# Performance work log

Hardware: AMD Instinct MI355X
Metric: run time of the kernel (lower is better)

## Reference

```python
import jax, jax.numpy as jnp
import numpy as np

N = 100000   # nodes
E = 625000   # edges
H = 128      # hidden dim
G = 64       # graphs in batch
HOPS = 5
EPS = 1e-5


def _gelu(x):
    return jax.nn.gelu(x, approximate=False)  # torch nn.GELU default (exact erf)


def _bn(x, g, b):
    # BatchNorm1d in training mode: batch statistics, biased variance
    m = jnp.mean(x, axis=0)
    v = jnp.var(x, axis=0)
    return (x - m) * jax.lax.rsqrt(v + EPS) * g + b


def _ffnn(x, W1, b1, W2, b2):
    # Linear -> GELU -> Linear -> GELU
    return _gelu(_gelu(x @ W1 + b1) @ W2 + b2)


def _vn_mlp(x, W1, b1, g1, be1, W2, b2, g2, be2):
    # Linear -> BN -> GELU -> Linear -> BN -> GELU
    h = _gelu(_bn(x @ W1 + b1, g1, be1))
    return _gelu(_bn(h @ W2 + b2, g2, be2))


def _gcn(x, W, b, src, dst):
    # PyG GCNConv: xW, symmetric-normalized aggregation over edges w/ self loops, + bias
    h = x @ W
    deg = jax.ops.segment_sum(jnp.ones_like(src, dtype=h.dtype), dst, num_segments=N)
    dinv = jax.lax.rsqrt(jnp.maximum(deg, 1.0))  # deg >= 1 due to self loops
    norm = dinv[src] * dinv[dst]                 # [E+N]
    out = jax.ops.segment_sum(h[src] * norm[:, None], dst, num_segments=N)
    return out + b


def _forward(x, edge_index, batch, pre_W1, pre_b1, pre_W2, pre_b2, conv_W, conv_b,
             bn_g, bn_b, ffn_W1, ffn_b1, ffn_W2, ffn_b2, vn_W1, vn_b1, vn_g1, vn_be1,
             vn_W2, vn_b2, vn_g2, vn_be2, vn_emb, post_W1, post_b1, post_W2, post_b2):
    loop = jnp.arange(N)
    src = jnp.concatenate([edge_index[0], loop])
    dst = jnp.concatenate([edge_index[1], loop])

    x = _ffnn(x.astype(jnp.float32), pre_W1, pre_b1, pre_W2, pre_b2)
    vn = jnp.broadcast_to(vn_emb[0], (G, H))  # vn(zeros(num_graphs))

    counts = jax.ops.segment_sum(jnp.ones((N,), x.dtype), batch, num_segments=G)
    inv_counts = 1.0 / jnp.maximum(counts, 1.0)

    for i in range(HOPS):
        x = x + vn[batch]
        x = _gcn(x, conv_W[i], conv_b[i], src, dst) + x
        x = _bn(x, bn_g[i], bn_b[i])
        x = _ffnn(x, ffn_W1[i], ffn_b1[i], ffn_W2[i], ffn_b2[i]) + x
        # dropout p=0.0 -> identity
        if i < HOPS - 1:
            pooled = jax.ops.segment_sum(x, batch, num_segments=G) * inv_counts[:, None]
            vn = vn + pooled
            vn = _vn_mlp(vn, vn_W1[i], vn_b1[i], vn_g1[i], vn_be1[i],
                         vn_W2[i], vn_b2[i], vn_g2[i], vn_be2[i])

    x = jax.ops.segment_sum(x, batch, num_segments=G)  # global_add_pool
    return _ffnn(x, post_W1, post_b1, post_W2, post_b2)


def setup_inputs():
    key = jax.random.key(0)
    ks = iter(jax.random.split(key, 40))
    def nrm(shape, s=0.05):
        return jax.random.normal(next(ks), shape, dtype=jnp.float32) * s
    d = {}
    d["x"] = jax.random.normal(next(ks), (N, H), dtype=jnp.float32)
    d["edge_index"] = jax.random.randint(next(ks), (2, E), 0, N)
    d["batch"] = jnp.sort(jax.random.randint(next(ks), (N,), 0, G))
    d["pre_W1"] = nrm((H, 2 * H)); d["pre_b1"] = jnp.zeros((2 * H,), jnp.float32)
    d["pre_W2"] = nrm((2 * H, H)); d["pre_b2"] = jnp.zeros((H,), jnp.float32)
    d["conv_W"] = nrm((HOPS, H, H)); d["conv_b"] = jnp.zeros((HOPS, H), jnp.float32)
    d["bn_g"] = jnp.ones((HOPS, H), jnp.float32); d["bn_b"] = jnp.zeros((HOPS, H), jnp.float32)
    d["ffn_W1"] = nrm((HOPS, H, 2 * H)); d["ffn_b1"] = jnp.zeros((HOPS, 2 * H), jnp.float32)
    d["ffn_W2"] = nrm((HOPS, 2 * H, H)); d["ffn_b2"] = jnp.zeros((HOPS, H), jnp.float32)
    d["vn_W1"] = nrm((HOPS - 1, H, 2 * H)); d["vn_b1"] = jnp.zeros((HOPS - 1, 2 * H), jnp.float32)
    d["vn_g1"] = jnp.ones((HOPS - 1, 2 * H), jnp.float32); d["vn_be1"] = jnp.zeros((HOPS - 1, 2 * H), jnp.float32)
    d["vn_W2"] = nrm((HOPS - 1, 2 * H, H)); d["vn_b2"] = jnp.zeros((HOPS - 1, H), jnp.float32)
    d["vn_g2"] = jnp.ones((HOPS - 1, H), jnp.float32); d["vn_be2"] = jnp.zeros((HOPS - 1, H), jnp.float32)
    d["vn_emb"] = nrm((1, H))
    d["post_W1"] = nrm((H, 2 * H)); d["post_b1"] = jnp.zeros((2 * H,), jnp.float32)
    d["post_W2"] = nrm((2 * H, H)); d["post_b2"] = jnp.zeros((H,), jnp.float32)
    return d


def reference(x, edge_index, batch, pre_W1, pre_b1, pre_W2, pre_b2, conv_W, conv_b,
              bn_g, bn_b, ffn_W1, ffn_b1, ffn_W2, ffn_b2, vn_W1, vn_b1, vn_g1, vn_be1,
              vn_W2, vn_b2, vn_g2, vn_be2, vn_emb, post_W1, post_b1, post_W2, post_b2):
    return _forward(x, edge_index, batch, pre_W1, pre_b1, pre_W2, pre_b2, conv_W, conv_b,
                    bn_g, bn_b, ffn_W1, ffn_b1, ffn_W2, ffn_b2, vn_W1, vn_b1, vn_g1, vn_be1,
                    vn_W2, vn_b2, vn_g2, vn_be2, vn_emb, post_W1, post_b1, post_W2, post_b2)
```

## Files before the change

kernel.cpp:

```cpp
#include <hip/hip_runtime.h>
#include <math.h>

#define H 128
#define H2 256
#define LDK 72
#define LDC 136
#define LDHW 136
#define FFN_SMEM (H2 * LDK)

typedef __attribute__((ext_vector_type(8))) short short8;
typedef __attribute__((ext_vector_type(4))) float floatx4;

__device__ __forceinline__ float gelu_f(float x) {
  float t = 1.59576912161f * x * fmaf(0.044715f, x * x, 1.0f);
  return x / (1.0f + __expf(-t));
}

__device__ __forceinline__ unsigned short f2b(float f) {
  union { float f; unsigned u; } c; c.f = f;
  unsigned r = c.u + 0x7fffu + ((c.u >> 16) & 1u);
  return (unsigned short)(r >> 16);
}

__device__ __forceinline__ float b2f(unsigned short u) {
  union { unsigned u; float f; } c; c.u = ((unsigned)u) << 16; return c.f;
}

__device__ __forceinline__ short8 pack8(floatx4 a, floatx4 b) {
  union { short8 v; unsigned short s[8]; } u;
  u.s[0] = f2b(a.x); u.s[1] = f2b(a.y); u.s[2] = f2b(a.z); u.s[3] = f2b(a.w);
  u.s[4] = f2b(b.x); u.s[5] = f2b(b.y); u.s[6] = f2b(b.z); u.s[7] = f2b(b.w);
  return u.v;
}

__global__ __launch_bounds__(256) void transpose_w(const float* __restrict__ W, unsigned short* __restrict__ WT,
                                                   int K, int Ncol, int total) {
  int i = blockIdx.x * 256 + threadIdx.x;
  if (i >= total) return;
  int kn = K * Ncol;
  int b = i / kn, r = i - b * kn;
  int k = r / Ncol, n = r - k * Ncol;
  WT[b * kn + n * K + k] = f2b(W[i]);
}


__global__ __launch_bounds__(256) void hist_kernel(int* __restrict__ cnt, const int* __restrict__ dst, int E) {
  int i = blockIdx.x * 256 + threadIdx.x;
  if (i < E) atomicAdd(&cnt[dst[i]], 1);
}

__global__ __launch_bounds__(256) void scan_a(const int* __restrict__ cnt, int* __restrict__ row_ptr,
                                              int* __restrict__ blockSum, float* __restrict__ dinv, int N) {
  __shared__ int ls[256];
  int t = threadIdx.x;
  int idx = blockIdx.x * 1024 + t * 4;
  int4 v = make_int4(0, 0, 0, 0);
  if (idx + 3 < N) v = *(const int4*)&cnt[idx];
  else {
    if (idx + 0 < N) v.x = cnt[idx + 0];
    if (idx + 1 < N) v.y = cnt[idx + 1];
    if (idx + 2 < N) v.z = cnt[idx + 2];
    if (idx + 3 < N) v.w = cnt[idx + 3];
  }
  if (idx + 0 < N) dinv[idx + 0] = rsqrtf((float)v.x + 1.0f);
  if (idx + 1 < N) dinv[idx + 1] = rsqrtf((float)v.y + 1.0f);
  if (idx + 2 < N) dinv[idx + 2] = rsqrtf((float)v.z + 1.0f);
  if (idx + 3 < N) dinv[idx + 3] = rsqrtf((float)v.w + 1.0f);
  int s = v.x + v.y + v.z + v.w;
  ls[t] = s;
  __syncthreads();
  for (int off = 1; off < 256; off <<= 1) {
    int a = (t >= off) ? ls[t - off] : 0;
    __syncthreads();
    ls[t] += a;
    __syncthreads();
  }
  int p = ls[t] - s;
  if (t == 255) blockSum[blockIdx.x] = ls[255];
  if (idx + 0 < N) row_ptr[idx + 0] = p;  p += v.x;
  if (idx + 1 < N) row_ptr[idx + 1] = p;  p += v.y;
  if (idx + 2 < N) row_ptr[idx + 2] = p;  p += v.z;
  if (idx + 3 < N) row_ptr[idx + 3] = p;
}

__global__ __launch_bounds__(1024) void scan_b(const int* __restrict__ blockSum, int* __restrict__ blockOff,
                                               int nb, int* __restrict__ row_ptr, int N, int E) {
  __shared__ int ls[1024];
  int t = threadIdx.x;
  int s = (t < nb) ? blockSum[t] : 0;
  ls[t] = s;
  __syncthreads();
  for (int off = 1; off < 1024; off <<= 1) {
    int a = (t >= off) ? ls[t - off] : 0;
    __syncthreads();
    ls[t] += a;
    __syncthreads();
  }
  if (t < nb) blockOff[t] = ls[t] - s;
  if (t == 0) row_ptr[N] = E;
}

__global__ __launch_bounds__(256) void scan_c(int* __restrict__ row_ptr, const int* __restrict__ blockOff, int N) {
  int t = threadIdx.x;
  int idx = blockIdx.x * 1024 + t * 4;
  int off = blockOff[blockIdx.x];
  if (off == 0) return;
  if (idx + 3 < N) {
    int4 v = *(const int4*)&row_ptr[idx];
    v.x += off; v.y += off; v.z += off; v.w += off;
    *(int4*)&row_ptr[idx] = v;
  } else {
    if (idx + 0 < N) row_ptr[idx + 0] += off;
    if (idx + 1 < N) row_ptr[idx + 1] += off;
    if (idx + 2 < N) row_ptr[idx + 2] += off;
    if (idx + 3 < N) row_ptr[idx + 3] += off;
  }
}

__global__ __launch_bounds__(256) void build_csr_kernel(const int* __restrict__ src, const int* __restrict__ dst,
                                                        const int* __restrict__ row_ptr, int* __restrict__ cursor,
                                                        const float* __restrict__ dinv,
                                                        int* __restrict__ csr_src, float* __restrict__ csr_norm,
                                                        int E) {
  int i = blockIdx.x * 256 + threadIdx.x;
  if (i < E) {
    int s = src[i], d = dst[i];
    int pos = row_ptr[d] + atomicAdd(&cursor[d], 1);
    csr_src[pos] = s;
    csr_norm[pos] = dinv[s] * dinv[d];
  }
}


__global__ __launch_bounds__(256) void count_kernel(float* counts, const int* __restrict__ batch, int N, int G) {
  __shared__ float hist[256];
  int t = threadIdx.x;
  if (t < G) hist[t] = 0.f;
  __syncthreads();
  int i0 = (blockIdx.x * 256 + t) * 16;
  int cur = -1; float run = 0.f;
  for (int j = 0; j < 16; j++) {
    int i = i0 + j;
    if (i < N) {
      int b = batch[i];
      if (b == cur) run += 1.f;
      else { if (cur >= 0) atomicAdd(&hist[cur], run); cur = b; run = 1.f; }
    }
  }
  if (cur >= 0) atomicAdd(&hist[cur], run);
  __syncthreads();
  if (t < G && hist[t] != 0.f) atomicAdd(&counts[t], hist[t]);
}

__global__ __launch_bounds__(256) void vn_init_kernel(float* vn, const float* __restrict__ emb, int n) {
  int i = blockIdx.x * 256 + threadIdx.x;
  if (i < n) vn[i] = emb[i & (H - 1)];
}

__global__ __launch_bounds__(256) void gather_agg(const unsigned short* __restrict__ h, const int* __restrict__ csr_src,
                                                  const float* __restrict__ csr_norm, const int* __restrict__ row_ptr,
                                                  const float* __restrict__ dinv, const float* __restrict__ vn,
                                                  const int* __restrict__ batch, const float* __restrict__ bias,
                                                  float* __restrict__ x, float* __restrict__ stats, int N) {
  __shared__ float sred[4 * H];
  __shared__ float qred[4 * H];
  int w = threadIdx.x >> 6, lane = threadIdx.x & 63;
  int c = lane * 2;
  float2 bi = *(const float2*)&bias[c];
  float s0t = 0.f, s1t = 0.f, q0t = 0.f, q1t = 0.f;
  int base = blockIdx.x * 32 + w * 8;
  for (int j = 0; j < 8; j++) {
    int node = base + j;
    if (node >= N) break;
    int b = batch[node];
    float di = dinv[node];
    float2 xo = *(const float2*)&x[(long)node * H + c];
    float2 vv = *(const float2*)&vn[b * H + c];
    unsigned hv = *(const unsigned*)&h[(long)node * H + c];
    int beg = row_ptr[node], end = row_ptr[node + 1];
    float ax = b2f((unsigned short)hv) * di * di;
    float ay = b2f((unsigned short)(hv >> 16)) * di * di;
    for (int e = beg; e < end; e += 8) {
      int si[8]; float wg[8]; unsigned u[8];
#pragma unroll
      for (int i = 0; i < 8; i++) {
        int ee = e + i;
        bool in = ee < end;
        int idx = in ? ee : beg;
        si[i] = csr_src[idx];
        wg[i] = in ? csr_norm[idx] : 0.f;
      }
#pragma unroll
      for (int i = 0; i < 8; i++) u[i] = *(const unsigned*)&h[(long)si[i] * H + c];
#pragma unroll
      for (int i = 0; i < 8; i++) {
        ax += b2f((unsigned short)u[i]) * wg[i];
        ay += b2f((unsigned short)(u[i] >> 16)) * wg[i];
      }
    }
    float rx = ax + xo.x + vv.x + bi.x;
    float ry = ay + xo.y + vv.y + bi.y;
    *(float2*)&x[(long)node * H + c] = make_float2(rx, ry);
    s0t += rx; q0t += rx * rx;
    s1t += ry; q1t += ry * ry;
  }
  sred[w * H + c] = s0t; sred[w * H + c + 1] = s1t;
  qred[w * H + c] = q0t; qred[w * H + c + 1] = q1t;
  __syncthreads();
  int t = threadIdx.x;
  if (t < H) {
    float s = sred[t] + sred[H + t] + sred[2 * H + t] + sred[3 * H + t];
    if (s != 0.f) atomicAdd(&stats[t], s);
  } else {
    int cc = t - H;
    float q = qred[cc] + qred[H + cc] + qred[2 * H + cc] + qred[3 * H + cc];
    if (q != 0.f) atomicAdd(&stats[H + cc], q);
  }
}

__global__ __launch_bounds__(128) void bn_finalize_kernel(const float* __restrict__ stats, const float* __restrict__ g,
                                                          const float* __restrict__ b, float* __restrict__ scsh,
                                                          float invN) {
  int c = threadIdx.x;
  float m = stats[c] * invN;
  float v = stats[H + c] * invN - m * m;
  float sc = rsqrtf(v + 1e-5f) * g[c];
  scsh[c] = sc;
  scsh[H + c] = b[c] - m * sc;
}

__global__ __launch_bounds__(256) void pool_kernel(float* __restrict__ pooled, const float* __restrict__ x,
                                                   const int* __restrict__ batch, int N) {
  int c = threadIdx.x & 127;
  int slab = threadIdx.x >> 7;
  int r0 = blockIdx.x * 128 + slab;
  float acc = 0.f;
  int cur = -1;
  for (int k = 0; k < 64; k++) {
    int r = r0 + k * 2;
    if (r >= N) break;
    int b = batch[r];
    if (b != cur) {
      if (cur >= 0) atomicAdd(&pooled[cur * H + c], acc);
      cur = b; acc = 0.f;
    }
    acc += x[(long)r * H + c];
  }
  if (cur >= 0) atomicAdd(&pooled[cur * H + c], acc);
}

__global__ __launch_bounds__(256) void conv_gemm(const float* __restrict__ x, const unsigned short* __restrict__ BT,
                                                 const float* __restrict__ vn, const int* __restrict__ batch,
                                                 unsigned short* __restrict__ h16, int M) {
  __shared__ unsigned short Bs[H * LDC];
  int tid = threadIdx.x;
  int lane = tid & 63, w = tid >> 6;
  int row0 = blockIdx.x * 64;
  int mrow = lane & 15, quad = lane >> 4, cn = lane & 15;
  int arow = row0 + w * 16 + mrow;
  bool rin = arow < M;
  int b = rin ? batch[arow] : 0;

#pragma unroll
  for (int j = 0; j < 8; j++) {
    int chunk = j * 256 + tid;
    int n = chunk >> 4, k8 = (chunk & 15) * 8;
    *(short8*)&Bs[n * LDC + k8] = *(const short8*)&BT[(long)n * H + k8];
  }

  short8 af[4];
#pragma unroll
  for (int k0 = 0; k0 < 4; k0++) {
    int kb = k0 * 32 + quad * 8;
    floatx4 a0 = (floatx4)0.f, a1 = (floatx4)0.f;
    if (rin) {
      a0 = *(const floatx4*)&x[(long)arow * H + kb] + *(const floatx4*)&vn[b * H + kb];
      a1 = *(const floatx4*)&x[(long)arow * H + kb + 4] + *(const floatx4*)&vn[b * H + kb + 4];
    }
    af[k0] = pack8(a0, a1);
  }
  __syncthreads();

#pragma unroll
  for (int t = 0; t < 8; t++) {
    floatx4 a = (floatx4)0.f;
#pragma unroll
    for (int k0 = 0; k0 < 4; k0++) {
      int kb = k0 * 32 + quad * 8;
      short8 bf = *(const short8*)&Bs[(t * 16 + mrow) * LDC + kb];
      a = __builtin_amdgcn_mfma_f32_16x16x32_bf16(af[k0], bf, a, 0, 0, 0);
    }
    int c = t * 16 + cn;
#pragma unroll
    for (int i = 0; i < 4; i++) {
      int r = row0 + w * 16 + quad * 4 + i;
      if (r < M) h16[(long)r * H + c] = f2b(a[i]);
    }
  }
}

template <int BNRES>
__global__ __launch_bounds__(256) void ffn_fused(const float* __restrict__ A,
                                                 const unsigned short* __restrict__ W1T, const float* __restrict__ b1,
                                                 const unsigned short* __restrict__ W2T, const float* __restrict__ b2,
                                                 const float* __restrict__ scsh,
                                                 float* __restrict__ C, int M) {
  __shared__ unsigned short smem[FFN_SMEM];
  unsigned short* Bs1 = smem;
  unsigned short* Bs2 = smem + 4 * 16 * LDHW;

  int tid = threadIdx.x;
  int lane = tid & 63, w = tid >> 6;
  unsigned short* HsW = smem + w * 16 * LDHW;
  int row0 = blockIdx.x * 64;
  int mrow = lane & 15, quad = lane >> 4, cn = lane & 15;
  int arow = row0 + w * 16 + mrow;
  bool rin = arow < M;

  short8 af[4];
#pragma unroll
  for (int k0 = 0; k0 < 4; k0++) {
    int kb = k0 * 32 + quad * 8;
    floatx4 a0 = (floatx4)0.f, a1 = (floatx4)0.f;
    if (rin) {
      a0 = *(const floatx4*)&A[(long)arow * H + kb];
      a1 = *(const floatx4*)&A[(long)arow * H + kb + 4];
      if (BNRES) {
        a0 = a0 * *(const floatx4*)&scsh[kb] + *(const floatx4*)&scsh[H + kb];
        a1 = a1 * *(const floatx4*)&scsh[kb + 4] + *(const floatx4*)&scsh[H + kb + 4];
      }
    }
    af[k0] = pack8(a0, a1);
  }

  floatx4 acc1[16];
#pragma unroll
  for (int t = 0; t < 16; t++) acc1[t] = (floatx4)0.f;

  for (int ks = 0; ks < 2; ks++) {
    if (ks > 0) __syncthreads();
#pragma unroll
    for (int j = 0; j < 8; j++) {
      int chunk = j * 256 + tid;
      int n = chunk >> 3, k8 = (chunk & 7) * 8;
      *(short8*)&Bs1[n * LDK + k8] = *(const short8*)&W1T[(long)n * H + ks * 64 + k8];
    }
    __syncthreads();
#pragma unroll
    for (int t = 0; t < 16; t++) {
      int kb = quad * 8;
      short8 bf0 = *(const short8*)&Bs1[(t * 16 + mrow) * LDK + kb];
      acc1[t] = __builtin_amdgcn_mfma_f32_16x16x32_bf16(af[ks * 2], bf0, acc1[t], 0, 0, 0);
      short8 bf1 = *(const short8*)&Bs1[(t * 16 + mrow) * LDK + 32 + kb];
      acc1[t] = __builtin_amdgcn_mfma_f32_16x16x32_bf16(af[ks * 2 + 1], bf1, acc1[t], 0, 0, 0);
    }
  }
  __syncthreads();

  short8 hf[8];
#pragma unroll
  for (int half = 0; half < 2; half++) {
#pragma unroll
    for (int t = 0; t < 8; t++) {
      int tt = half * 8 + t;
      int cg = tt * 16 + cn;
      int cl = t * 16 + cn;
      float bb = b1[cg];
#pragma unroll
      for (int i = 0; i < 4; i++) {
        int r = quad * 4 + i;
        HsW[r * LDHW + cl] = f2b(gelu_f(acc1[tt][i] + bb));
      }
    }
#pragma unroll
    for (int k0 = 0; k0 < 4; k0++)
      hf[half * 4 + k0] = *(const short8*)&HsW[mrow * LDHW + k0 * 32 + quad * 8];
  }

#pragma unroll
  for (int j = 0; j < 4; j++) {
    int chunk = j * 256 + tid;
    int n = chunk >> 3, k8 = (chunk & 7) * 8;
    *(short8*)&Bs2[n * LDK + k8] = *(const short8*)&W2T[(long)n * H2 + k8];
  }
  __syncthreads();

  floatx4 acc2[8];
#pragma unroll
  for (int t = 0; t < 8; t++) acc2[t] = (floatx4)0.f;

  for (int ks = 0; ks < 4; ks++) {
    if (ks > 0) {
      __syncthreads();
#pragma unroll
      for (int j = 0; j < 4; j++) {
        int chunk = j * 256 + tid;
        int n = chunk >> 3, k8 = (chunk & 7) * 8;
        *(short8*)&Bs2[n * LDK + k8] = *(const short8*)&W2T[(long)n * H2 + ks * 64 + k8];
      }
      __syncthreads();
    }
    int kk = ks * 2;
#pragma unroll
    for (int t = 0; t < 8; t++) {
      int kb0 = quad * 8;
      short8 bf0 = *(const short8*)&Bs2[(t * 16 + mrow) * LDK + kb0];
      acc2[t] = __builtin_amdgcn_mfma_f32_16x16x32_bf16(hf[kk], bf0, acc2[t], 0, 0, 0);
      short8 bf1 = *(const short8*)&Bs2[(t * 16 + mrow) * LDK + 32 + kb0];
      acc2[t] = __builtin_amdgcn_mfma_f32_16x16x32_bf16(hf[kk + 1], bf1, acc2[t], 0, 0, 0);
    }
  }

#pragma unroll
  for (int t = 0; t < 8; t++) {
    int c = t * 16 + cn;
    float bb = b2[c];
    float rsc = 0.f, rsh = 0.f;
    if (BNRES) { rsc = scsh[c]; rsh = scsh[H + c]; }
#pragma unroll
    for (int i = 0; i < 4; i++) {
      int r = row0 + w * 16 + quad * 4 + i;
      if (r < M) {
        long off = (long)r * H + c;
        float v = gelu_f(acc2[t][i] + bb);
        if (BNRES) v += C[off] * rsc + rsh;
        C[off] = v;
      }
    }
  }
}

template <int BN, int UVN>
__global__ __launch_bounds__(256) void mlp64_l1(const float* __restrict__ vn, const float* __restrict__ pooled,
                                                const float* __restrict__ counts,
                                                const float* __restrict__ W1, const float* __restrict__ b1,
                                                const float* __restrict__ g1, const float* __restrict__ be1,
                                                float* __restrict__ h1) {
  __shared__ float u[64 * H];
  __shared__ float red[8 * 64];
  int t = threadIdx.x;
  for (int idx = t; idx < 64 * H; idx += 256) {
    float v = pooled[idx];
    if (UVN) v = vn[idx] + v / fmaxf(counts[idx >> 7], 1.0f);
    u[idx] = v;
  }
  __syncthreads();
  int tc = t & 63, tg = t >> 6;
  int c = blockIdx.x * 64 + tc;
  float acc[16];
  float bj = b1[c];
#pragma unroll
  for (int g = 0; g < 16; g++) acc[g] = bj;
  for (int k0 = 0; k0 < H; k0 += 4) {
    float w0 = W1[(k0 + 0) * H2 + c];
    float w1 = W1[(k0 + 1) * H2 + c];
    float w2 = W1[(k0 + 2) * H2 + c];
    float w3 = W1[(k0 + 3) * H2 + c];
#pragma unroll
    for (int g = 0; g < 16; g++) {
      float4 v = *(const float4*)&u[(tg * 16 + g) * H + k0];
      acc[g] += v.x * w0 + v.y * w1 + v.z * w2 + v.w * w3;
    }
  }
  float sc = 1.f, sh = 0.f;
  if (BN) {
    float s = 0.f, s2 = 0.f;
#pragma unroll
    for (int g = 0; g < 16; g++) { s += acc[g]; s2 += acc[g] * acc[g]; }
    red[tg * 64 + tc] = s;
    red[256 + tg * 64 + tc] = s2;
    __syncthreads();
    float st = red[tc] + red[64 + tc] + red[128 + tc] + red[192 + tc];
    float st2 = red[256 + tc] + red[320 + tc] + red[384 + tc] + red[448 + tc];
    float m = st * (1.f / 64.f);
    float var = st2 * (1.f / 64.f) - m * m;
    sc = rsqrtf(var + 1e-5f) * g1[c];
    sh = be1[c] - m * sc;
  }
#pragma unroll
  for (int g = 0; g < 16; g++) h1[(tg * 16 + g) * H2 + c] = gelu_f(acc[g] * sc + sh);
}

template <int BN>
__global__ __launch_bounds__(256) void mlp64_l2(const float* __restrict__ h1,
                                                const float* __restrict__ W2, const float* __restrict__ b2,
                                                const float* __restrict__ g2, const float* __restrict__ be2,
                                                float* __restrict__ outp) {
  __shared__ float red[8 * 64];
  int t = threadIdx.x;
  int tc = t & 63, tg = t >> 6;
  int c = blockIdx.x * 64 + tc;
  float acc[16];
  float bj = b2[c];
#pragma unroll
  for (int g = 0; g < 16; g++) acc[g] = bj;
  for (int k0 = 0; k0 < H2; k0 += 4) {
    float w0 = W2[(k0 + 0) * H + c];
    float w1 = W2[(k0 + 1) * H + c];
    float w2 = W2[(k0 + 2) * H + c];
    float w3 = W2[(k0 + 3) * H + c];
#pragma unroll
    for (int g = 0; g < 16; g++) {
      float4 v = *(const float4*)&h1[(tg * 16 + g) * H2 + k0];
      acc[g] += v.x * w0 + v.y * w1 + v.z * w2 + v.w * w3;
    }
  }
  float sc = 1.f, sh = 0.f;
  if (BN) {
    float s = 0.f, s2 = 0.f;
#pragma unroll
    for (int g = 0; g < 16; g++) { s += acc[g]; s2 += acc[g] * acc[g]; }
    red[tg * 64 + tc] = s;
    red[256 + tg * 64 + tc] = s2;
    __syncthreads();
    float st = red[tc] + red[64 + tc] + red[128 + tc] + red[192 + tc];
    float st2 = red[256 + tc] + red[320 + tc] + red[384 + tc] + red[448 + tc];
    float m = st * (1.f / 64.f);
    float var = st2 * (1.f / 64.f) - m * m;
    sc = rsqrtf(var + 1e-5f) * g2[c];
    sh = be2[c] - m * sc;
  }
#pragma unroll
  for (int g = 0; g < 16; g++) outp[(tg * 16 + g) * H + c] = gelu_f(acc[g] * sc + sh);
}


extern "C" void kernel_launch(void* const* d_in, const int* in_sizes, int n_in,
                              void* d_out, int out_size, void* d_ws, size_t ws_size,
                              hipStream_t stream) {
  const float* x_in   = (const float*)d_in[0];
  const int*   edge   = (const int*)d_in[1];
  const int*   batch  = (const int*)d_in[2];
  const float* pre_W1 = (const float*)d_in[3];
  const float* pre_b1 = (const float*)d_in[4];
  const float* pre_W2 = (const float*)d_in[5];
  const float* pre_b2 = (const float*)d_in[6];
  const float* conv_W = (const float*)d_in[7];
  const float* conv_b = (const float*)d_in[8];
  const float* bn_g   = (const float*)d_in[9];
  const float* bn_b   = (const float*)d_in[10];
  const float* ffn_W1 = (const float*)d_in[11];
  const float* ffn_b1 = (const float*)d_in[12];
  const float* ffn_W2 = (const float*)d_in[13];
  const float* ffn_b2 = (const float*)d_in[14];
  const float* vn_W1  = (const float*)d_in[15];
  const float* vn_b1  = (const float*)d_in[16];
  const float* vn_g1  = (const float*)d_in[17];
  const float* vn_be1 = (const float*)d_in[18];
  const float* vn_W2  = (const float*)d_in[19];
  const float* vn_b2  = (const float*)d_in[20];
  const float* vn_g2  = (const float*)d_in[21];
  const float* vn_be2 = (const float*)d_in[22];
  const float* vn_emb = (const float*)d_in[23];
  const float* post_W1= (const float*)d_in[24];
  const float* post_b1= (const float*)d_in[25];
  const float* post_W2= (const float*)d_in[26];
  const float* post_b2= (const float*)d_in[27];
  float* out = (float*)d_out;

  const int N    = in_sizes[2];
  const int E    = in_sizes[1] / 2;
  const int G    = out_size / H;
  const int HOPS = in_sizes[7] / (H * H);
  const int NH   = N * H;

  float* w = (float*)d_ws;
  float* buf_x  = w;  w += NH;
  float* buf_t  = w;  w += N * H2;
  unsigned short* buf_h16 = (unsigned short*)buf_t;
  float* dinv   = w;  w += N;
  float* counts = w;  w += G;
  float* stats  = w;  w += 2 * H;
  float* scsh   = w;  w += 2 * H;
  float* pooled = w;  w += G * H;
  float* vn     = w;  w += G * H;
  float* mlp_h1 = w;  w += G * H2;
  float* csr_norm = w; w += E;
  int* iw = (int*)w;
  int* cnt      = iw;  iw += N;
  int* row_ptr  = iw;  iw += N + 1;
  int* cursor   = iw;  iw += N;
  int* csr_src  = iw;  iw += E;
  int* blockSum = iw;  iw += 1024;
  int* blockOff = iw;  iw += 1024;
  unsigned short* wt = (unsigned short*)iw;
  unsigned short* preW1T = wt;  wt += H * H2;
  unsigned short* preW2T = wt;  wt += H2 * H;
  unsigned short* convT  = wt;  wt += HOPS * H * H;
  unsigned short* ffn1T  = wt;  wt += HOPS * H * H2;
  unsigned short* ffn2T  = wt;  wt += HOPS * H2 * H;

  const int* src = edge;
  const int* dst = edge + E;

  int gE  = (E + 255) / 256;
  int gM  = (N + 63) / 64;
  int nb  = (N + 1023) / 1024;
  float invN = 1.0f / (float)N;

  transpose_w<<<(H * H2 + 255) / 256, 256, 0, stream>>>(pre_W1, preW1T, H, H2, H * H2);
  transpose_w<<<(H2 * H + 255) / 256, 256, 0, stream>>>(pre_W2, preW2T, H2, H, H2 * H);
  transpose_w<<<(HOPS * H * H + 255) / 256, 256, 0, stream>>>(conv_W, convT, H, H, HOPS * H * H);
  transpose_w<<<(HOPS * H * H2 + 255) / 256, 256, 0, stream>>>(ffn_W1, ffn1T, H, H2, HOPS * H * H2);
  transpose_w<<<(HOPS * H2 * H + 255) / 256, 256, 0, stream>>>(ffn_W2, ffn2T, H2, H, HOPS * H2 * H);

  hipMemsetAsync(cnt, 0, N * sizeof(int), stream);
  hist_kernel<<<gE, 256, 0, stream>>>(cnt, dst, E);
  scan_a<<<nb, 256, 0, stream>>>(cnt, row_ptr, blockSum, dinv, N);
  scan_b<<<1, 1024, 0, stream>>>(blockSum, blockOff, nb, row_ptr, N, E);
  scan_c<<<nb, 256, 0, stream>>>(row_ptr, blockOff, N);
  hipMemsetAsync(cursor, 0, N * sizeof(int), stream);
  build_csr_kernel<<<gE, 256, 0, stream>>>(src, dst, row_ptr, cursor, dinv, csr_src, csr_norm, E);

  hipMemsetAsync(counts, 0, G * sizeof(float), stream);
  count_kernel<<<(N + 256 * 16 - 1) / (256 * 16), 256, 0, stream>>>(counts, batch, N, G);
  vn_init_kernel<<<(G * H + 255) / 256, 256, 0, stream>>>(vn, vn_emb, G * H);

  ffn_fused<0><<<gM, 256, 0, stream>>>(x_in, preW1T, pre_b1, preW2T, pre_b2, nullptr, buf_x, N);

  for (int i = 0; i < HOPS; i++) {
    conv_gemm<<<gM, 256, 0, stream>>>(buf_x, convT + i * H * H, vn, batch, buf_h16, N);
    hipMemsetAsync(stats, 0, 2 * H * sizeof(float), stream);
    gather_agg<<<(N + 31) / 32, 256, 0, stream>>>(buf_h16, csr_src, csr_norm, row_ptr, dinv, vn, batch,
                                                  conv_b + i * H, buf_x, stats, N);
    bn_finalize_kernel<<<1, 128, 0, stream>>>(stats, bn_g + i * H, bn_b + i * H, scsh, invN);
    ffn_fused<1><<<gM, 256, 0, stream>>>(buf_x, ffn1T + i * H * H2, ffn_b1 + i * H2,
                                         ffn2T + i * H2 * H, ffn_b2 + i * H, scsh, buf_x, N);
    if (i < HOPS - 1) {
      hipMemsetAsync(pooled, 0, G * H * sizeof(float), stream);
      pool_kernel<<<(N + 127) / 128, 256, 0, stream>>>(pooled, buf_x, batch, N);
      mlp64_l1<1, 1><<<H2 / 64, 256, 0, stream>>>(vn, pooled, counts,
                                                  vn_W1 + i * H * H2, vn_b1 + i * H2, vn_g1 + i * H2, vn_be1 + i * H2,
                                                  mlp_h1);
      mlp64_l2<1><<<H / 64, 256, 0, stream>>>(mlp_h1, vn_W2 + i * H2 * H, vn_b2 + i * H, vn_g2 + i * H, vn_be2 + i * H, vn);
    }
  }

  hipMemsetAsync(pooled, 0, G * H * sizeof(float), stream);
  pool_kernel<<<(N + 127) / 128, 256, 0, stream>>>(pooled, buf_x, batch, N);
  mlp64_l1<0, 0><<<H2 / 64, 256, 0, stream>>>(nullptr, pooled, nullptr, post_W1, post_b1, nullptr, nullptr, mlp_h1);
  mlp64_l2<0><<<H / 64, 256, 0, stream>>>(mlp_h1, post_W2, post_b2, nullptr, nullptr, out);
}
```

Baseline: 1.877 ms.

## Make FFN kernel persistent with resident weights and fused graph pooling

Replaces the per-tile FFN kernel with a persistent 1024-thread kernel that loads both weight matrices into LDS once per block. Each wave then loops over 16-row tiles, computing the first GEMM in column pairs and feeding the GELU output straight into the second GEMM through a small per-wave scratch area. Graph mean-pooling is folded into the FFN epilogue using shuffle reductions and atomics, which removes the separate pool kernel and its re-read of x. The costs are a large LDS footprint that limits each CU to one block, and more atomics when a tile spans two graphs.

```diff
diff --git a/kernel.cpp b/kernel.cpp
--- a/kernel.cpp
+++ b/kernel.cpp
@@ -3,10 +3,7 @@
 
 #define H 128
 #define H2 256
-#define LDK 72
 #define LDC 136
-#define LDHW 136
-#define FFN_SMEM (H2 * LDK)
 
 typedef __attribute__((ext_vector_type(8))) short short8;
 typedef __attribute__((ext_vector_type(4))) float floatx4;
@@ -229,26 +226,6 @@
   scsh[H + c] = b[c] - m * sc;
 }
 
-__global__ __launch_bounds__(256) void pool_kernel(float* __restrict__ pooled, const float* __restrict__ x,
-                                                   const int* __restrict__ batch, int N) {
-  int c = threadIdx.x & 127;
-  int slab = threadIdx.x >> 7;
-  int r0 = blockIdx.x * 128 + slab;
-  float acc = 0.f;
-  int cur = -1;
-  for (int k = 0; k < 64; k++) {
-    int r = r0 + k * 2;
-    if (r >= N) break;
-    int b = batch[r];
-    if (b != cur) {
-      if (cur >= 0) atomicAdd(&pooled[cur * H + c], acc);
-      cur = b; acc = 0.f;
-    }
-    acc += x[(long)r * H + c];
-  }
-  if (cur >= 0) atomicAdd(&pooled[cur * H + c], acc);
-}
-
 __global__ __launch_bounds__(256) void conv_gemm(const float* __restrict__ x, const unsigned short* __restrict__ BT,
                                                  const float* __restrict__ vn, const int* __restrict__ batch,
                                                  unsigned short* __restrict__ h16, int M) {
@@ -299,132 +276,114 @@
   }
 }
 
-template <int BNRES>
-__global__ __launch_bounds__(256) void ffn_fused(const float* __restrict__ A,
-                                                 const unsigned short* __restrict__ W1T, const float* __restrict__ b1,
-                                                 const unsigned short* __restrict__ W2T, const float* __restrict__ b2,
-                                                 const float* __restrict__ scsh,
-                                                 float* __restrict__ C, int M) {
-  __shared__ unsigned short smem[FFN_SMEM];
-  unsigned short* Bs1 = smem;
-  unsigned short* Bs2 = smem + 4 * 16 * LDHW;
-
+template <int BNRES, int POOL>
+__global__ __launch_bounds__(1024) void ffn_persist(const float* __restrict__ A,
+                                                    const unsigned short* __restrict__ W1T, const float* __restrict__ b1,
+                                                    const unsigned short* __restrict__ W2T, const float* __restrict__ b2,
+                                                    const float* __restrict__ scsh,
+                                                    float* __restrict__ C, float* __restrict__ pooled,
+                                                    const int* __restrict__ batch, int M) {
+  __shared__ unsigned short lds[78848];
   int tid = threadIdx.x;
+#pragma unroll
+  for (int j = 0; j < 4; j++) {
+    int idx = j * 1024 + tid;
+    int n = idx >> 4, k8 = (idx & 15) * 8;
+    *(short8*)&lds[n * 136 + k8] = *(const short8*)&W1T[n * 128 + k8];
+  }
+#pragma unroll
+  for (int j = 0; j < 4; j++) {
+    int idx = j * 1024 + tid;
+    int n = idx >> 5, k8 = (idx & 31) * 8;
+    *(short8*)&lds[34816 + n * 264 + k8] = *(const short8*)&W2T[n * 256 + k8];
+  }
+  __syncthreads();
+
   int lane = tid & 63, w = tid >> 6;
-  unsigned short* HsW = smem + w * 16 * LDHW;
-  int row0 = blockIdx.x * 64;
   int mrow = lane & 15, quad = lane >> 4, cn = lane & 15;
-  int arow = row0 + w * 16 + mrow;
-  bool rin = arow < M;
-
-  short8 af[4];
-#pragma unroll
-  for (int k0 = 0; k0 < 4; k0++) {
-    int kb = k0 * 32 + quad * 8;
-    floatx4 a0 = (floatx4)0.f, a1 = (floatx4)0.f;
-    if (rin) {
-      a0 = *(const floatx4*)&A[(long)arow * H + kb];
-      a1 = *(const floatx4*)&A[(long)arow * H + kb + 4];
-      if (BNRES) {
-        a0 = a0 * *(const floatx4*)&scsh[kb] + *(const floatx4*)&scsh[H + kb];
-        a1 = a1 * *(const floatx4*)&scsh[kb + 4] + *(const floatx4*)&scsh[H + kb + 4];
+  unsigned short* scr = &lds[68608 + w * 640];
+  int TT = (M + 15) >> 4;
+  int stride = (int)(gridDim.x << 4);
+
+  for (int tile = blockIdx.x * 16 + w; tile < TT; tile += stride) {
+    int row0 = tile << 4;
+    int arow = row0 + mrow;
+    bool rin = arow < M;
+
+    short8 af[4];
+#pragma unroll
+    for (int k0 = 0; k0 < 4; k0++) {
+      int kb = k0 * 32 + quad * 8;
+      floatx4 a0 = (floatx4)0.f, a1 = (floatx4)0.f;
+      if (rin) {
+        a0 = *(const floatx4*)&A[(long)arow * H + kb];
+        a1 = *(const floatx4*)&A[(long)arow * H + kb + 4];
+        if (BNRES) {
+          a0 = a0 * *(const floatx4*)&scsh[kb] + *(const floatx4*)&scsh[H + kb];
+          a1 = a1 * *(const floatx4*)&scsh[kb + 4] + *(const floatx4*)&scsh[H + kb + 4];
+        }
       }
-    }
-    af[k0] = pack8(a0, a1);
-  }
-
-  floatx4 acc1[16];
-#pragma unroll
-  for (int t = 0; t < 16; t++) acc1[t] = (floatx4)0.f;
-
-  for (int ks = 0; ks < 2; ks++) {
-    if (ks > 0) __syncthreads();
-#pragma unroll
-    for (int j = 0; j < 8; j++) {
-      int chunk = j * 256 + tid;
-      int n = chunk >> 3, k8 = (chunk & 7) * 8;
-      *(short8*)&Bs1[n * LDK + k8] = *(const short8*)&W1T[(long)n * H + ks * 64 + k8];
-    }
-    __syncthreads();
-#pragma unroll
-    for (int t = 0; t < 16; t++) {
-      int kb = quad * 8;
-      short8 bf0 = *(const short8*)&Bs1[(t * 16 + mrow) * LDK + kb];
-      acc1[t] = __builtin_amdgcn_mfma_f32_16x16x32_bf16(af[ks * 2], bf0, acc1[t], 0, 0, 0);
-      short8 bf1 = *(const short8*)&Bs1[(t * 16 + mrow) * LDK + 32 + kb];
-      acc1[t] = __builtin_amdgcn_mfma_f32_16x16x32_bf16(af[ks * 2 + 1], bf1, acc1[t], 0, 0, 0);
-    }
-  }
-  __syncthreads();
-
-  short8 hf[8];
-#pragma unroll
-  for (int half = 0; half < 2; half++) {
+      af[k0] = pack8(a0, a1);
+    }
+
+    floatx4 acc2[8];
+#pragma unroll
+    for (int t = 0; t < 8; t++) acc2[t] = (floatx4)0.f;
+
+#pragma unroll
+    for (int p = 0; p < 8; p++) {
+#pragma unroll
+      for (int u = 0; u < 2; u++) {
+        int t = p * 2 + u;
+        floatx4 a = (floatx4)0.f;
+#pragma unroll
+        for (int k = 0; k < 4; k++) {
+          short8 bf = *(const short8*)&lds[(t * 16 + mrow) * 136 + k * 32 + quad * 8];
+          a = __builtin_amdgcn_mfma_f32_16x16x32_bf16(af[k], bf, a, 0, 0, 0);
+        }
+        float bb = b1[t * 16 + cn];
+#pragma unroll
+        for (int i = 0; i < 4; i++)
+          scr[(quad * 4 + i) * 40 + u * 16 + cn] = f2b(gelu_f(a[i] + bb));
+      }
+      short8 hf = *(const short8*)&scr[mrow * 40 + quad * 8];
+#pragma unroll
+      for (int ct = 0; ct < 8; ct++) {
+        short8 bf = *(const short8*)&lds[34816 + (ct * 16 + mrow) * 264 + p * 32 + quad * 8];
+        acc2[ct] = __builtin_amdgcn_mfma_f32_16x16x32_bf16(hf, bf, acc2[ct], 0, 0, 0);
+      }
+    }
+
+    int g0 = 0; bool same = true;
+    if (POOL) {
+      int rl = row0 + 15; if (rl >= M) rl = M - 1;
+      g0 = batch[row0];
+      same = (batch[rl] == g0);
+    }
 #pragma unroll
     for (int t = 0; t < 8; t++) {
-      int tt = half * 8 + t;
-      int cg = tt * 16 + cn;
-      int cl = t * 16 + cn;
-      float bb = b1[cg];
+      int c = t * 16 + cn;
+      float bb = b2[c];
+      float rsc = 0.f, rsh = 0.f;
+      if (BNRES) { rsc = scsh[c]; rsh = scsh[H + c]; }
+      float s = 0.f;
 #pragma unroll
       for (int i = 0; i < 4; i++) {
-        int r = quad * 4 + i;
-        HsW[r * LDHW + cl] = f2b(gelu_f(acc1[tt][i] + bb));
+        int r = row0 + quad * 4 + i;
+        float v = 0.f;
+        if (r < M) {
+          long off = (long)r * H + c;
+          v = gelu_f(acc2[t][i] + bb);
+          if (BNRES) v += C[off] * rsc + rsh;
+          C[off] = v;
+          if (POOL && !same) atomicAdd(&pooled[batch[r] * H + c], v);
+        }
+        s += v;
       }
-    }
-#pragma unroll
-    for (int k0 = 0; k0 < 4; k0++)
-      hf[half * 4 + k0] = *(const short8*)&HsW[mrow * LDHW + k0 * 32 + quad * 8];
-  }
-
-#pragma unroll
-  for (int j = 0; j < 4; j++) {
-    int chunk = j * 256 + tid;
-    int n = chunk >> 3, k8 = (chunk & 7) * 8;
-    *(short8*)&Bs2[n * LDK + k8] = *(const short8*)&W2T[(long)n * H2 + k8];
-  }
-  __syncthreads();
-
-  floatx4 acc2[8];
-#pragma unroll
-  for (int t = 0; t < 8; t++) acc2[t] = (floatx4)0.f;
-
-  for (int ks = 0; ks < 4; ks++) {
-    if (ks > 0) {
-      __syncthreads();
-#pragma unroll
-      for (int j = 0; j < 4; j++) {
-        int chunk = j * 256 + tid;
-        int n = chunk >> 3, k8 = (chunk & 7) * 8;
-        *(short8*)&Bs2[n * LDK + k8] = *(const short8*)&W2T[(long)n * H2 + ks * 64 + k8];
-      }
-      __syncthreads();
-    }
-    int kk = ks * 2;
-#pragma unroll
-    for (int t = 0; t < 8; t++) {
-      int kb0 = quad * 8;
-      short8 bf0 = *(const short8*)&Bs2[(t * 16 + mrow) * LDK + kb0];
-      acc2[t] = __builtin_amdgcn_mfma_f32_16x16x32_bf16(hf[kk], bf0, acc2[t], 0, 0, 0);
-      short8 bf1 = *(const short8*)&Bs2[(t * 16 + mrow) * LDK + 32 + kb0];
-      acc2[t] = __builtin_amdgcn_mfma_f32_16x16x32_bf16(hf[kk + 1], bf1, acc2[t], 0, 0, 0);
-    }
-  }
-
-#pragma unroll
-  for (int t = 0; t < 8; t++) {
-    int c = t * 16 + cn;
-    float bb = b2[c];
-    float rsc = 0.f, rsh = 0.f;
-    if (BNRES) { rsc = scsh[c]; rsh = scsh[H + c]; }
-#pragma unroll
-    for (int i = 0; i < 4; i++) {
-      int r = row0 + w * 16 + quad * 4 + i;
-      if (r < M) {
-        long off = (long)r * H + c;
-        float v = gelu_f(acc2[t][i] + bb);
-        if (BNRES) v += C[off] * rsc + rsh;
-        C[off] = v;
+      if (POOL && same) {
+        s += __shfl_xor(s, 16);
+        s += __shfl_xor(s, 32);
+        if (quad == 0) atomicAdd(&pooled[g0 * H + c], s);
       }
     }
   }
@@ -616,7 +575,8 @@
   count_kernel<<<(N + 256 * 16 - 1) / (256 * 16), 256, 0, stream>>>(counts, batch, N, G);
   vn_init_kernel<<<(G * H + 255) / 256, 256, 0, stream>>>(vn, vn_emb, G * H);
 
-  ffn_fused<0><<<gM, 256, 0, stream>>>(x_in, preW1T, pre_b1, preW2T, pre_b2, nullptr, buf_x, N);
+  ffn_persist<0, 0><<<256, 1024, 0, stream>>>(x_in, preW1T, pre_b1, preW2T, pre_b2, nullptr,
+                                              buf_x, nullptr, nullptr, N);
 
   for (int i = 0; i < HOPS; i++) {
     conv_gemm<<<gM, 256, 0, stream>>>(buf_x, convT + i * H * H, vn, batch, buf_h16, N);
@@ -624,11 +584,11 @@
     gather_agg<<<(N + 31) / 32, 256, 0, stream>>>(buf_h16, csr_src, csr_norm, row_ptr, dinv, vn, batch,
                                                   conv_b + i * H, buf_x, stats, N);
     bn_finalize_kernel<<<1, 128, 0, stream>>>(stats, bn_g + i * H, bn_b + i * H, scsh, invN);
-    ffn_fused<1><<<gM, 256, 0, stream>>>(buf_x, ffn1T + i * H * H2, ffn_b1 + i * H2,
-                                         ffn2T + i * H2 * H, ffn_b2 + i * H, scsh, buf_x, N);
+    hipMemsetAsync(pooled, 0, G * H * sizeof(float), stream);
+    ffn_persist<1, 1><<<256, 1024, 0, stream>>>(buf_x, ffn1T + i * H * H2, ffn_b1 + i * H2,
+                                                ffn2T + i * H2 * H, ffn_b2 + i * H, scsh,
+                                                buf_x, pooled, batch, N);
     if (i < HOPS - 1) {
-      hipMemsetAsync(pooled, 0, G * H * sizeof(float), stream);
-      pool_kernel<<<(N + 127) / 128, 256, 0, stream>>>(pooled, buf_x, batch, N);
       mlp64_l1<1, 1><<<H2 / 64, 256, 0, stream>>>(vn, pooled, counts,
                                                   vn_W1 + i * H * H2, vn_b1 + i * H2, vn_g1 + i * H2, vn_be1 + i * H2,
                                                   mlp_h1);
@@ -636,8 +596,6 @@
     }
   }
 
-  hipMemsetAsync(pooled, 0, G * H * sizeof(float), stream);
-  pool_kernel<<<(N + 127) / 128, 256, 0, stream>>>(pooled, buf_x, batch, N);
   mlp64_l1<0, 0><<<H2 / 64, 256, 0, stream>>>(nullptr, pooled, nullptr, post_W1, post_b1, nullptr, nullptr, mlp_h1);
   mlp64_l2<0><<<H / 64, 256, 0, stream>>>(mlp_h1, post_W2, post_b2, nullptr, nullptr, out);
 }
```

Result: faster. 1.778 ms (-5.3%).
